# Performance work log

Measured on AMD Instinct MI355X. Metric: run time of the kernel, lower is better.

## Reference

```python
import jax, jax.numpy as jnp
import numpy as np
from jax import lax

A_PLUS = 0.01
A_MINUS = 0.01
TAU_PLUS = 20.0
TAU_MINUS = 20.0
W_MAX = 1.0
W_MIN = 0.0

B, T, PRE_N, POST_N = 16, 128, 2048, 2048


def setup_inputs() -> dict:
    key = jax.random.key(0)
    k1, k2, k3 = jax.random.split(key, 3)
    weights = jax.random.uniform(k1, (POST_N, PRE_N), dtype=jnp.float32)
    pre_spikes = jax.random.uniform(k2, (B, T, PRE_N), dtype=jnp.float32)
    post_spikes = jax.random.uniform(k3, (B, T, POST_N), dtype=jnp.float32)
    return {"weights": weights, "pre_spikes": pre_spikes,
            "post_spikes": post_spikes, "dt": 1}


def compute_trace(spikes, tau, dt):
    # Faithful to torch loop: trace[:,0,:] = 0; trace[t] = decay*trace[t-1] + spikes[t] for t>=1
    decay = jnp.exp(jnp.float32(-dt / tau))
    s_tb = jnp.swapaxes(spikes, 0, 1)  # [T, B, N]
    init = jnp.zeros_like(s_tb[0])

    def step(carry, s_t):
        tr = decay * carry + s_t
        return tr, tr

    _, tr = lax.scan(step, init, s_tb[1:])          # [T-1, B, N]
    tr = jnp.concatenate([init[None], tr], axis=0)  # [T, B, N]
    return jnp.swapaxes(tr, 0, 1)                   # [B, T, N]


def reference(weights, pre_spikes, post_spikes, dt):
    batch = pre_spikes.shape[0]
    pre_trace = compute_trace(pre_spikes, TAU_PLUS, dt)
    post_trace = compute_trace(post_spikes, TAU_MINUS, dt)

    # sum over t of mean over batch of outer products -> single contraction over (b, t)
    # ltp[q,p] = A_plus * sum_t mean_b post_spikes[b,t,q] * pre_trace[b,t,p]
    ltp = A_PLUS * jnp.einsum('btq,btp->qp', post_spikes, pre_trace) / batch
    # ltd[q,p] = -A_minus * sum_t mean_b post_trace[b,t,q] * pre_spikes[b,t,p]
    ltd = -A_MINUS * jnp.einsum('btq,btp->qp', post_trace, pre_spikes) / batch

    # softbound weight dependence (constant in t, distributes over the sum)
    w_factor = (W_MAX - weights) * (weights - W_MIN) / ((W_MAX - W_MIN) / 2) ** 2
    delta_w = w_factor * (ltp + ltd)
    return delta_w
```

## Files before the change

### kernel.cpp

```cpp
#include <hip/hip_runtime.h>
#include <hip/hip_bf16.h>


typedef __attribute__((ext_vector_type(8))) short bf16x8;
typedef __attribute__((ext_vector_type(4))) float f32x4;

#define GN 2048
#define KTOT 2048
#define A_SCALE (0.01f / 16.0f)
#define FST 68
#define ZST 66

#define GLOAD_LDS16(gp, lp) \
    __builtin_amdgcn_global_load_lds((const __attribute__((address_space(1))) void*)(gp), \
                                     (__attribute__((address_space(3))) void*)(lp), 16, 0, 0)

__device__ __forceinline__ unsigned bf16bits(float x) {
    __hip_bfloat16 h = __float2bfloat16(x);
    return (unsigned)*(unsigned short*)&h;
}

__global__ __launch_bounds__(256, 4) void trace_kernel(
    const float* __restrict__ pre,
    const float* __restrict__ post,
    const int* __restrict__ dtp,
    __hip_bfloat16* __restrict__ AT,
    __hip_bfloat16* __restrict__ BT)
{
    __shared__ float fbuf[128 * FST];
    __hip_bfloat16* zbuf = (__hip_bfloat16*)fbuf;

    const int tid = threadIdx.x;
    const int w   = tid >> 6;
    const int l   = tid & 63;
    const int nq  = tid & 15;
    const int tl  = tid >> 4;
    const int n0  = blockIdx.x * 64;
    const int b   = blockIdx.y;
    const int a   = blockIdx.z;

    int di = dtp[0];
    float dtf = (di > 0 && di < 1000000) ? (float)di : *(const float*)dtp;
    const float decay = __expf(-dtf / 20.0f);

    if (a == 0) {
        #pragma unroll
        for (int pass = 0; pass < 8; ++pass) {
            const int t = pass * 16 + tl;
            float4 v = *(const float4*)&post[((size_t)b * 128 + t) * GN + n0 + 4 * nq];
            uint2 pk;
            pk.x = bf16bits(v.x) | (bf16bits(v.y) << 16);
            pk.y = bf16bits(v.z) | (bf16bits(v.w) << 16);
            *(uint2*)&zbuf[t * ZST + 4 * nq] = pk;
        }
        __syncthreads();
    } else {
        #pragma unroll
        for (int pass = 0; pass < 8; ++pass) {
            const int t = pass * 16 + tl;
            float4 v = *(const float4*)&pre[((size_t)b * 128 + t) * GN + n0 + 4 * nq];
            *(float4*)&fbuf[t * FST + 4 * nq] = v;
        }
        __syncthreads();

        const int t0 = 32 * w;
        float carry = 0.0f;
        #pragma unroll 8
        for (int t = 1; t < t0; ++t)
            carry = decay * carry + fbuf[t * FST + l];
        float z[32];
        #pragma unroll
        for (int j = 0; j < 32; ++j) {
            const int t = t0 + j;
            if (t >= 1) carry = decay * carry + fbuf[t * FST + l];
            z[j] = carry;
        }
        float bc = 0.0f;
        #pragma unroll 8
        for (int t = 127; t >= t0 + 32; --t)
            bc = decay * bc + fbuf[t * FST + l];
        #pragma unroll
        for (int j = 31; j >= 0; --j) {
            const int t = t0 + j;
            bc = decay * bc + fbuf[t * FST + l];
            if (t >= 1) z[j] -= bc;
        }
        __syncthreads();
        #pragma unroll
        for (int j = 0; j < 32; ++j)
            zbuf[(t0 + j) * ZST + l] = __float2bfloat16(z[j]);
        __syncthreads();
    }

    __hip_bfloat16* dst = (a == 0) ? AT : BT;
    #pragma unroll
    for (int j = 0; j < 4; ++j) {
        const int c  = tid + 256 * j;
        const int n  = c >> 4;
        const int tc = c & 15;
        unsigned int vv[8];
        #pragma unroll
        for (int i = 0; i < 8; ++i)
            vv[i] = *(const unsigned short*)&zbuf[(8 * tc + i) * ZST + n];
        uint4 pk;
        pk.x = vv[0] | (vv[1] << 16);
        pk.y = vv[2] | (vv[3] << 16);
        pk.z = vv[4] | (vv[5] << 16);
        pk.w = vv[6] | (vv[7] << 16);
        *(uint4*)(dst + (size_t)(n0 + n) * KTOT + b * 128 + tc * 8) = pk;
    }
}

__global__ __launch_bounds__(256) void stdp_gemm(
    const __hip_bfloat16* __restrict__ AT,
    const __hip_bfloat16* __restrict__ BT,
    const float* __restrict__ W,
    float* __restrict__ out)
{
    __shared__ alignas(16) __hip_bfloat16 As[128 * 64];
    __shared__ alignas(16) __hip_bfloat16 Bs[64 * 64];

    const int tid  = threadIdx.x;
    const int lane = tid & 63;
    const int wv   = tid >> 6;
    const int wm   = (wv >> 1) * 64;
    const int wn   = (wv & 1) * 32;
    const int RM   = blockIdx.y * 128;
    const int CN   = blockIdx.x * 64;
    const int l15  = lane & 15;
    const int quad = lane >> 4;

    f32x4 acc[4][2] = {};

    for (int k0 = 0; k0 < KTOT; k0 += 64) {
        __syncthreads();
        #pragma unroll
        for (int it = 0; it < 4; ++it) {
            const int cbase = it * 256 + wv * 64;
            const int c     = cbase + lane;
            const int row   = c >> 3;
            const int kc    = (c & 7) ^ (row & 7);
            GLOAD_LDS16(AT + (size_t)(RM + row) * KTOT + k0 + kc * 8, As + (size_t)cbase * 8);
        }
        #pragma unroll
        for (int it = 0; it < 2; ++it) {
            const int cbase = it * 256 + wv * 64;
            const int c     = cbase + lane;
            const int row   = c >> 3;
            const int kc    = (c & 7) ^ (row & 7);
            GLOAD_LDS16(BT + (size_t)(CN + row) * KTOT + k0 + kc * 8, Bs + (size_t)cbase * 8);
        }
        __syncthreads();

        #pragma unroll
        for (int kk = 0; kk < 64; kk += 32) {
            const int jg = (kk >> 3) + quad;
            bf16x8 af[4], bfr[2];
            #pragma unroll
            for (int i = 0; i < 4; ++i) {
                const int mr = wm + i * 16 + l15;
                af[i] = *(const bf16x8*)(As + mr * 64 + ((jg ^ (mr & 7)) * 8));
            }
            #pragma unroll
            for (int j = 0; j < 2; ++j) {
                const int nr = wn + j * 16 + l15;
                bfr[j] = *(const bf16x8*)(Bs + nr * 64 + ((jg ^ (nr & 7)) * 8));
            }
            #pragma unroll
            for (int i = 0; i < 4; ++i)
                #pragma unroll
                for (int j = 0; j < 2; ++j)
                    acc[i][j] = __builtin_amdgcn_mfma_f32_16x16x32_bf16(
                        af[i], bfr[j], acc[i][j], 0, 0, 0);
        }
    }

    #pragma unroll
    for (int i = 0; i < 4; ++i) {
        #pragma unroll
        for (int r = 0; r < 4; ++r) {
            const int q = RM + wm + i * 16 + quad * 4 + r;
            #pragma unroll
            for (int j = 0; j < 2; ++j) {
                const int p = CN + wn + j * 16 + l15;
                const float w  = W[(size_t)q * GN + p];
                const float wf = 4.0f * w * (1.0f - w);
                out[(size_t)q * GN + p] = wf * A_SCALE * acc[i][j][r];
            }
        }
    }
}

extern "C" void kernel_launch(void* const* d_in, const int* in_sizes, int n_in,
                              void* d_out, int out_size, void* d_ws, size_t ws_size,
                              hipStream_t stream) {
    const float* W    = (const float*)d_in[0];
    const float* pre  = (const float*)d_in[1];
    const float* post = (const float*)d_in[2];
    const int*   dt   = (const int*)d_in[3];
    float* out = (float*)d_out;

    __hip_bfloat16* AT = (__hip_bfloat16*)d_ws;
    __hip_bfloat16* BT = AT + (size_t)GN * KTOT;

    trace_kernel<<<dim3(32, 16, 2), 256, 0, stream>>>(pre, post, dt, AT, BT);
    stdp_gemm<<<dim3(32, 16), 256, 0, stream>>>(AT, BT, W, out);
}
```

Measured before the change: 125.6 us.

## Split GEMM K dimension across two wave groups with LDS reduction

Doubles the GEMM block to 512 threads, with two 4-wave groups each handling half of the K=2048 reduction in separate LDS buffers. At the end, group 1 writes its partial accumulators to shared memory and group 0 adds them before applying the softbound weight factor and storing. The goal is more waves in flight per tile to hide load latency, since the grid has only 512 blocks. In exchange it uses more LDS per block, adds an extra reduction step with two barriers, and halves the epilogue parallelism.

```diff
diff --git a/kernel.cpp b/kernel.cpp
--- a/kernel.cpp
+++ b/kernel.cpp
@@ -10,6 +10,7 @@
 #define A_SCALE (0.01f / 16.0f)
 #define FST 68
 #define ZST 66
+#define RST 36
 
 #define GLOAD_LDS16(gp, lp) \
     __builtin_amdgcn_global_load_lds((const __attribute__((address_space(1))) void*)(gp), \
@@ -111,18 +112,19 @@
     }
 }
 
-__global__ __launch_bounds__(256) void stdp_gemm(
+__global__ __launch_bounds__(512) void stdp_gemm(
     const __hip_bfloat16* __restrict__ AT,
     const __hip_bfloat16* __restrict__ BT,
     const float* __restrict__ W,
     float* __restrict__ out)
 {
-    __shared__ alignas(16) __hip_bfloat16 As[128 * 64];
-    __shared__ alignas(16) __hip_bfloat16 Bs[64 * 64];
+    __shared__ alignas(16) char smem[49152];
 
     const int tid  = threadIdx.x;
     const int lane = tid & 63;
-    const int wv   = tid >> 6;
+    const int wv8  = tid >> 6;
+    const int grp  = wv8 >> 2;
+    const int wv   = wv8 & 3;
     const int wm   = (wv >> 1) * 64;
     const int wn   = (wv & 1) * 32;
     const int RM   = blockIdx.y * 128;
@@ -130,9 +132,13 @@
     const int l15  = lane & 15;
     const int quad = lane >> 4;
 
+    __hip_bfloat16* Ag = (__hip_bfloat16*)(smem + grp * 24576);
+    __hip_bfloat16* Bg = (__hip_bfloat16*)(smem + grp * 24576 + 16384);
+
     f32x4 acc[4][2] = {};
 
-    for (int k0 = 0; k0 < KTOT; k0 += 64) {
+    const int K0 = grp * 1024;
+    for (int k0 = K0; k0 < K0 + 1024; k0 += 64) {
         __syncthreads();
         #pragma unroll
         for (int it = 0; it < 4; ++it) {
@@ -140,7 +146,7 @@
             const int c     = cbase + lane;
             const int row   = c >> 3;
             const int kc    = (c & 7) ^ (row & 7);
-            GLOAD_LDS16(AT + (size_t)(RM + row) * KTOT + k0 + kc * 8, As + (size_t)cbase * 8);
+            GLOAD_LDS16(AT + (size_t)(RM + row) * KTOT + k0 + kc * 8, Ag + (size_t)cbase * 8);
         }
         #pragma unroll
         for (int it = 0; it < 2; ++it) {
@@ -148,7 +154,7 @@
             const int c     = cbase + lane;
             const int row   = c >> 3;
             const int kc    = (c & 7) ^ (row & 7);
-            GLOAD_LDS16(BT + (size_t)(CN + row) * KTOT + k0 + kc * 8, Bs + (size_t)cbase * 8);
+            GLOAD_LDS16(BT + (size_t)(CN + row) * KTOT + k0 + kc * 8, Bg + (size_t)cbase * 8);
         }
         __syncthreads();
 
@@ -159,12 +165,12 @@
             #pragma unroll
             for (int i = 0; i < 4; ++i) {
                 const int mr = wm + i * 16 + l15;
-                af[i] = *(const bf16x8*)(As + mr * 64 + ((jg ^ (mr & 7)) * 8));
+                af[i] = *(const bf16x8*)(Ag + mr * 64 + ((jg ^ (mr & 7)) * 8));
             }
             #pragma unroll
             for (int j = 0; j < 2; ++j) {
                 const int nr = wn + j * 16 + l15;
-                bfr[j] = *(const bf16x8*)(Bs + nr * 64 + ((jg ^ (nr & 7)) * 8));
+                bfr[j] = *(const bf16x8*)(Bg + nr * 64 + ((jg ^ (nr & 7)) * 8));
             }
             #pragma unroll
             for (int i = 0; i < 4; ++i)
@@ -175,17 +181,34 @@
         }
     }
 
-    #pragma unroll
-    for (int i = 0; i < 4; ++i) {
-        #pragma unroll
-        for (int r = 0; r < 4; ++r) {
-            const int q = RM + wm + i * 16 + quad * 4 + r;
-            #pragma unroll
-            for (int j = 0; j < 2; ++j) {
-                const int p = CN + wn + j * 16 + l15;
-                const float w  = W[(size_t)q * GN + p];
-                const float wf = 4.0f * w * (1.0f - w);
-                out[(size_t)q * GN + p] = wf * A_SCALE * acc[i][j][r];
+    float* red = (float*)smem;
+    const int rbase = wv * 64 * RST;
+    __syncthreads();
+    if (grp == 1) {
+        #pragma unroll
+        for (int i = 0; i < 4; ++i)
+            #pragma unroll
+            for (int r = 0; r < 4; ++r)
+                #pragma unroll
+                for (int j = 0; j < 2; ++j)
+                    red[rbase + (i * 16 + quad * 4 + r) * RST + j * 16 + l15] = acc[i][j][r];
+    }
+    __syncthreads();
+    if (grp == 0) {
+        #pragma unroll
+        for (int i = 0; i < 4; ++i) {
+            #pragma unroll
+            for (int r = 0; r < 4; ++r) {
+                const int q = RM + wm + i * 16 + quad * 4 + r;
+                #pragma unroll
+                for (int j = 0; j < 2; ++j) {
+                    const int p = CN + wn + j * 16 + l15;
+                    float v = acc[i][j][r]
+                            + red[rbase + (i * 16 + quad * 4 + r) * RST + j * 16 + l15];
+                    const float w  = W[(size_t)q * GN + p];
+                    const float wf = 4.0f * w * (1.0f - w);
+                    out[(size_t)q * GN + p] = wf * A_SCALE * v;
+                }
             }
         }
     }
@@ -204,5 +227,5 @@
     __hip_bfloat16* BT = AT + (size_t)GN * KTOT;
 
     trace_kernel<<<dim3(32, 16, 2), 256, 0, stream>>>(pre, post, dt, AT, BT);
-    stdp_gemm<<<dim3(32, 16), 256, 0, stream>>>(AT, BT, W, out);
-}
+    stdp_gemm<<<dim3(32, 16), 512, 0, stream>>>(AT, BT, W, out);
+}
```

After: 121.1 us. 1.04x faster.
